# Optimization experiments

Measured on AMD Instinct MI355X. Metric: run time of the kernel, lower is better.

Reference implementation:

```python
import jax, jax.numpy as jnp
import numpy as np

N_NODES = 50000
N_EDGES = 640000
D_IN = 128
D_H1 = 128
D_H2 = 128
N_CLASSES = 64


def setup_inputs() -> dict:
    key = jax.random.key(0)
    ks = jax.random.split(key, 8)
    x = jax.random.normal(ks[0], (N_NODES, D_IN), dtype=jnp.float32)
    edge_index = jax.random.randint(ks[1], (2, N_EDGES), 0, N_NODES, dtype=jnp.int64)
    s1 = 1.0 / np.sqrt(D_IN)
    s2 = 1.0 / np.sqrt(D_H1)
    s3 = 1.0 / np.sqrt(D_H2)
    W1 = jax.random.uniform(ks[2], (D_IN, D_H1), jnp.float32, -s1, s1)
    b1 = jnp.zeros((D_H1,), jnp.float32)
    W2 = jax.random.uniform(ks[3], (D_H1, D_H2), jnp.float32, -s2, s2)
    b2 = jnp.zeros((D_H2,), jnp.float32)
    Wl = jax.random.uniform(ks[4], (D_H2, N_CLASSES), jnp.float32, -s3, s3)
    bl = jax.random.uniform(ks[5], (N_CLASSES,), jnp.float32, -s3, s3)
    return {"x": x, "edge_index": edge_index, "W1": W1, "b1": b1,
            "W2": W2, "b2": b2, "Wl": Wl, "bl": bl}


def _gcn_norm(edge_index, num_nodes):
    # PyG GCNConv: add self-loops, symmetric normalization D^-1/2 (A+I) D^-1/2
    loop = jnp.arange(num_nodes, dtype=edge_index.dtype)
    src = jnp.concatenate([edge_index[0], loop])
    dst = jnp.concatenate([edge_index[1], loop])
    deg = jax.ops.segment_sum(jnp.ones_like(dst, dtype=jnp.float32), dst,
                              num_segments=num_nodes)
    dinv = jnp.where(deg > 0, jax.lax.rsqrt(deg), 0.0)
    norm = dinv[src] * dinv[dst]  # [E+N]
    return src, dst, norm


def _gcn_conv(h, src, dst, norm, W, b, num_nodes):
    h = h @ W                       # transform first (smaller gather when D_out small)
    msg = h[src] * norm[:, None]    # gather + per-edge scale  [E+N, D_out]
    agg = jax.ops.segment_sum(msg, dst, num_segments=num_nodes)  # scatter-add
    return agg + b


def reference(x, edge_index, W1, b1, W2, b2, Wl, bl):
    n = x.shape[0]
    src, dst, norm = _gcn_norm(edge_index, n)
    h = jax.nn.relu(_gcn_conv(x, src, dst, norm, W1, b1, n))
    # dropout is identity in eval mode
    h = jax.nn.relu(_gcn_conv(h, src, dst, norm, W2, b2, n))
    return h @ Wl + bl
```

## Files before the change

### kernel.cpp

```cpp
#include <hip/hip_runtime.h>


typedef __attribute__((ext_vector_type(8))) __bf16 bf16x8;
typedef __attribute__((ext_vector_type(8))) short short8;
typedef __attribute__((ext_vector_type(4))) float f32x4;

__device__ inline float bf_lo(unsigned u) { return __uint_as_float(u << 16); }
__device__ inline float bf_hi(unsigned u) { return __uint_as_float(u & 0xffff0000u); }
__device__ inline unsigned short f2bf(float v) {
  return __builtin_bit_cast(unsigned short, (__bf16)v);
}

__global__ void k_count(const int* __restrict__ dst, int E, int* __restrict__ cnt) {
  int i = blockIdx.x * blockDim.x + threadIdx.x;
  if (i < E) atomicAdd(&cnt[dst[i]], 1);
}

__global__ void k_scan1(const int* __restrict__ cnt, int n, int* __restrict__ partial) {
  __shared__ int s[256];
  int i = blockIdx.x * 256 + threadIdx.x;
  s[threadIdx.x] = (i < n) ? cnt[i] : 0;
  __syncthreads();
  for (int off = 128; off > 0; off >>= 1) {
    if (threadIdx.x < off) s[threadIdx.x] += s[threadIdx.x + off];
    __syncthreads();
  }
  if (threadIdx.x == 0) partial[blockIdx.x] = s[0];
}

__global__ void k_scan3(const int* __restrict__ cnt, const int* __restrict__ partial,
                        int nb, int n, int* __restrict__ row_off, int* __restrict__ cursor,
                        float* __restrict__ dinv) {
  __shared__ int s[256];
  __shared__ int base_s;
  int t = threadIdx.x;
  s[t] = (t < nb && t < (int)blockIdx.x) ? partial[t] : 0;
  __syncthreads();
  for (int off = 128; off > 0; off >>= 1) {
    if (t < off) s[t] += s[t + off];
    __syncthreads();
  }
  if (t == 0) base_s = s[0];
  __syncthreads();
  int base = base_s;
  __syncthreads();

  int i = blockIdx.x * 256 + t;
  int v = (i < n) ? cnt[i] : 0;
  s[t] = v;
  __syncthreads();
  for (int off = 1; off < 256; off <<= 1) {
    int u = (t >= off) ? s[t - off] : 0;
    __syncthreads();
    s[t] += u;
    __syncthreads();
  }
  int incl = s[t];
  int excl = incl - v;
  if (i < n) {
    row_off[i] = base + excl;
    cursor[i] = base + excl;
    dinv[i] = rsqrtf((float)(v + 1));
    if (i == n - 1) row_off[n] = base + incl;
  }
}

__global__ void k_place(const int* __restrict__ src, const int* __restrict__ dst, int E,
                        int* __restrict__ cursor, const float* __restrict__ dinv,
                        unsigned long long* __restrict__ edges) {
  int e = blockIdx.x * blockDim.x + threadIdx.x;
  if (e < E) {
    int s = src[e], d = dst[e];
    int pos = atomicAdd(&cursor[d], 1);
    unsigned long long packed =
        (unsigned long long)(unsigned)s |
        ((unsigned long long)__float_as_uint(dinv[s] * dinv[d]) << 32);
    __builtin_nontemporal_store(packed, &edges[pos]);
  }
}

__global__ void k_prepW(const float* __restrict__ W1, const float* __restrict__ W2,
                        const float* __restrict__ Wl,
                        unsigned short* __restrict__ b1h, unsigned short* __restrict__ b1l,
                        unsigned short* __restrict__ b2h, unsigned short* __restrict__ b2l,
                        unsigned short* __restrict__ blh, unsigned short* __restrict__ bll) {
  int idx = blockIdx.x * 256 + threadIdx.x;
  const float* W;
  unsigned short *bh, *bl_;
  int N, local;
  if (idx < 16384)      { W = W1; bh = b1h; bl_ = b1l; N = 128; local = idx; }
  else if (idx < 32768) { W = W2; bh = b2h; bl_ = b2l; N = 128; local = idx - 16384; }
  else if (idx < 40960) { W = Wl; bh = blh; bl_ = bll; N = 64;  local = idx - 32768; }
  else return;
  int n = local >> 7, k = local & 127;
  float v = W[(size_t)k * N + n];
  __bf16 h = (__bf16)v;
  bh[local] = __builtin_bit_cast(unsigned short, h);
  bl_[local] = f2bf(v - (float)h);
}

template <int NT, bool A32, bool BIAS, bool OUT_BF16>
__global__ __launch_bounds__(256) void gemm2(
    const void* __restrict__ Ahi_, const unsigned short* __restrict__ Alo,
    const unsigned short* __restrict__ Bhi, const unsigned short* __restrict__ Blo,
    const float* __restrict__ bias, void* __restrict__ Cout, int M) {
  constexpr int K = 128;
  constexpr int NCOL = NT * 16;
  __shared__ alignas(16) unsigned short lbh[NCOL * K];
  __shared__ alignas(16) unsigned short lbl[NCOL * K];
  int t = threadIdx.x;
  for (int c = t; c < NCOL * 16; c += 256) {
    int r = c >> 4, q = c & 15;
    int sq = q ^ (r & 15);
    *(short8*)&lbh[r * K + sq * 8] = *(const short8*)&Bhi[r * K + q * 8];
    *(short8*)&lbl[r * K + sq * 8] = *(const short8*)&Blo[r * K + q * 8];
  }
  __syncthreads();

  int lane = t & 63, wave = t >> 6;
  int lm = lane & 15, lk = lane >> 4;
  int m_base = blockIdx.x * 128 + wave * 32;

  f32x4 acc[2][NT] = {};
  const short8 zero8 = {0, 0, 0, 0, 0, 0, 0, 0};

#pragma unroll
  for (int ks = 0; ks < 4; ++ks) {
    int k0 = ks * 32 + lk * 8;
    int chunk = (ks * 4 + lk);
    bf16x8 bh[NT], bl[NT];
#pragma unroll
    for (int nt = 0; nt < NT; ++nt) {
      int r = nt * 16 + lm;
      int sq = chunk ^ lm;
      bh[nt] = *(const bf16x8*)&lbh[r * K + sq * 8];
      bl[nt] = *(const bf16x8*)&lbl[r * K + sq * 8];
    }
#pragma unroll
    for (int mt = 0; mt < 2; ++mt) {
      int row = m_base + mt * 16 + lm;
      bf16x8 ah, al;
      if (A32) {
        const float* Af = (const float*)Ahi_;
        if (row < M) {
          float4 v0 = *(const float4*)&Af[(size_t)row * K + k0];
          float4 v1 = *(const float4*)&Af[(size_t)row * K + k0 + 4];
          float a[8] = {v0.x, v0.y, v0.z, v0.w, v1.x, v1.y, v1.z, v1.w};
#pragma unroll
          for (int j = 0; j < 8; ++j) {
            __bf16 h = (__bf16)a[j];
            ah[j] = h;
            al[j] = (__bf16)(a[j] - (float)h);
          }
        } else {
          ah = __builtin_bit_cast(bf16x8, zero8);
          al = __builtin_bit_cast(bf16x8, zero8);
        }
      } else {
        const unsigned short* Ahi = (const unsigned short*)Ahi_;
        if (row < M) {
          ah = *(const bf16x8*)&Ahi[(size_t)row * K + k0];
          al = *(const bf16x8*)&Alo[(size_t)row * K + k0];
        } else {
          ah = __builtin_bit_cast(bf16x8, zero8);
          al = __builtin_bit_cast(bf16x8, zero8);
        }
      }
#pragma unroll
      for (int nt = 0; nt < NT; ++nt) {
        acc[mt][nt] = __builtin_amdgcn_mfma_f32_16x16x32_bf16(ah, bh[nt], acc[mt][nt], 0, 0, 0);
        acc[mt][nt] = __builtin_amdgcn_mfma_f32_16x16x32_bf16(ah, bl[nt], acc[mt][nt], 0, 0, 0);
        acc[mt][nt] = __builtin_amdgcn_mfma_f32_16x16x32_bf16(al, bh[nt], acc[mt][nt], 0, 0, 0);
      }
    }
  }

#pragma unroll
  for (int mt = 0; mt < 2; ++mt) {
#pragma unroll
    for (int r = 0; r < 4; ++r) {
      int row = m_base + mt * 16 + lk * 4 + r;
      if (row < M) {
#pragma unroll
        for (int nt = 0; nt < NT; ++nt) {
          int col = nt * 16 + lm;
          float v = acc[mt][nt][r];
          if (BIAS) v += bias[col];
          if (OUT_BF16)
            ((unsigned short*)Cout)[(size_t)row * NCOL + col] = f2bf(v);
          else
            ((float*)Cout)[(size_t)row * NCOL + col] = v;
        }
      }
    }
  }
}

__global__ __launch_bounds__(256) void k_agg(const unsigned short* __restrict__ t,
                      const int* __restrict__ row_off,
                      const int2* __restrict__ edges,
                      const float* __restrict__ dinv, const float* __restrict__ bias,
                      unsigned short* __restrict__ ghi, unsigned short* __restrict__ glo,
                      int n) {
  int wave = threadIdx.x >> 6;
  int lane = threadIdx.x & 63;
  int half = lane >> 5;
  int hl = lane & 31;
  int node = blockIdx.x * 4 + wave;
  if (node >= n) return;
  int e0 = row_off[node], e1 = row_off[node + 1];

  float4 a0 = {0,0,0,0}, a1 = {0,0,0,0}, a2 = {0,0,0,0}, a3 = {0,0,0,0};
  int e = e0 + half;
  for (; e + 6 < e1; e += 8) {
    int2 p0 = edges[e],     p1 = edges[e + 2];
    int2 p2 = edges[e + 4], p3 = edges[e + 6];
    uint2 u0 = *(const uint2*)&t[(size_t)p0.x * 128 + hl * 4];
    uint2 u1 = *(const uint2*)&t[(size_t)p1.x * 128 + hl * 4];
    uint2 u2 = *(const uint2*)&t[(size_t)p2.x * 128 + hl * 4];
    uint2 u3 = *(const uint2*)&t[(size_t)p3.x * 128 + hl * 4];
    float w0 = __int_as_float(p0.y), w1 = __int_as_float(p1.y);
    float w2 = __int_as_float(p2.y), w3 = __int_as_float(p3.y);
    a0.x += w0 * bf_lo(u0.x); a0.y += w0 * bf_hi(u0.x);
    a0.z += w0 * bf_lo(u0.y); a0.w += w0 * bf_hi(u0.y);
    a1.x += w1 * bf_lo(u1.x); a1.y += w1 * bf_hi(u1.x);
    a1.z += w1 * bf_lo(u1.y); a1.w += w1 * bf_hi(u1.y);
    a2.x += w2 * bf_lo(u2.x); a2.y += w2 * bf_hi(u2.x);
    a2.z += w2 * bf_lo(u2.y); a2.w += w2 * bf_hi(u2.y);
    a3.x += w3 * bf_lo(u3.x); a3.y += w3 * bf_hi(u3.x);
    a3.z += w3 * bf_lo(u3.y); a3.w += w3 * bf_hi(u3.y);
  }
  for (; e < e1; e += 2) {
    int2 p = edges[e];
    uint2 u = *(const uint2*)&t[(size_t)p.x * 128 + hl * 4];
    float w = __int_as_float(p.y);
    a0.x += w * bf_lo(u.x); a0.y += w * bf_hi(u.x);
    a0.z += w * bf_lo(u.y); a0.w += w * bf_hi(u.y);
  }
  float sx = (a0.x + a1.x) + (a2.x + a3.x);
  float sy = (a0.y + a1.y) + (a2.y + a3.y);
  float sz = (a0.z + a1.z) + (a2.z + a3.z);
  float sw = (a0.w + a1.w) + (a2.w + a3.w);
  sx += __shfl_xor(sx, 32);
  sy += __shfl_xor(sy, 32);
  sz += __shfl_xor(sz, 32);
  sw += __shfl_xor(sw, 32);
  if (half == 0) {
    float di = dinv[node];
    float self = di * di;
    uint2 sv = *(const uint2*)&t[(size_t)node * 128 + hl * 4];
    sx += self * bf_lo(sv.x); sy += self * bf_hi(sv.x);
    sz += self * bf_lo(sv.y); sw += self * bf_hi(sv.y);
    float4 bb = *(const float4*)&bias[hl * 4];
    sx = fmaxf(sx + bb.x, 0.f); sy = fmaxf(sy + bb.y, 0.f);
    sz = fmaxf(sz + bb.z, 0.f); sw = fmaxf(sw + bb.w, 0.f);
    __bf16 hx = (__bf16)sx, hy = (__bf16)sy, hz = (__bf16)sz, hw = (__bf16)sw;
    ushort4 ho, lo;
    ho.x = __builtin_bit_cast(unsigned short, hx);
    ho.y = __builtin_bit_cast(unsigned short, hy);
    ho.z = __builtin_bit_cast(unsigned short, hz);
    ho.w = __builtin_bit_cast(unsigned short, hw);
    lo.x = f2bf(sx - (float)hx);
    lo.y = f2bf(sy - (float)hy);
    lo.z = f2bf(sz - (float)hz);
    lo.w = f2bf(sw - (float)hw);
    *(ushort4*)&ghi[(size_t)node * 128 + hl * 4] = ho;
    *(ushort4*)&glo[(size_t)node * 128 + hl * 4] = lo;
  }
}

extern "C" void kernel_launch(void* const* d_in, const int* in_sizes, int n_in,
                              void* d_out, int out_size, void* d_ws, size_t ws_size,
                              hipStream_t stream) {
  const float* x  = (const float*)d_in[0];
  const int*   ei = (const int*)d_in[1];
  const float* W1 = (const float*)d_in[2];
  const float* b1 = (const float*)d_in[3];
  const float* W2 = (const float*)d_in[4];
  const float* b2 = (const float*)d_in[5];
  const float* Wl = (const float*)d_in[6];
  const float* bl = (const float*)d_in[7];
  float* out = (float*)d_out;

  const int D = 128;
  int N = in_sizes[0] / D;
  int E = in_sizes[1] / 2;
  const int* src = ei;
  const int* dst = ei + E;

  uintptr_t ws = (uintptr_t)d_ws;
  auto take = [&](size_t bytes) {
    uintptr_t p = ws;
    ws += (bytes + 15) & ~(size_t)15;
    return p;
  };
  unsigned short* t_bf = (unsigned short*)take((size_t)N * D * 2);
  unsigned short* xh   = (unsigned short*)take((size_t)N * D * 2);
  unsigned short* xl   = (unsigned short*)take((size_t)N * D * 2);
  unsigned long long* edges = (unsigned long long*)take((size_t)E * 8);
  int*   cnt     = (int*)take((size_t)N * sizeof(int));
  int*   row_off = (int*)take(((size_t)N + 1) * sizeof(int));
  int*   cursor  = (int*)take((size_t)N * sizeof(int));
  float* dinv    = (float*)take((size_t)N * sizeof(float));
  int*   partial = (int*)take(256 * sizeof(int));
  unsigned short* b1h = (unsigned short*)take(128 * 128 * 2);
  unsigned short* b1l = (unsigned short*)take(128 * 128 * 2);
  unsigned short* b2h = (unsigned short*)take(128 * 128 * 2);
  unsigned short* b2l = (unsigned short*)take(128 * 128 * 2);
  unsigned short* blh = (unsigned short*)take(128 * 64 * 2);
  unsigned short* bll = (unsigned short*)take(128 * 64 * 2);

  int nb_n = (N + 255) / 256;
  int nb_e = (E + 255) / 256;

  hipMemsetAsync(cnt, 0, (size_t)N * sizeof(int), stream);
  k_count<<<nb_e, 256, 0, stream>>>(dst, E, cnt);
  k_scan1<<<nb_n, 256, 0, stream>>>(cnt, N, partial);
  k_scan3<<<nb_n, 256, 0, stream>>>(cnt, partial, nb_n, N, row_off, cursor, dinv);
  k_place<<<nb_e, 256, 0, stream>>>(src, dst, E, cursor, dinv, edges);

  k_prepW<<<(40960 + 255) / 256, 256, 0, stream>>>(W1, W2, Wl, b1h, b1l, b2h, b2l, blh, bll);

  int gemm_blocks = (N + 127) / 128;
  int agg_blocks = (N + 3) / 4;

  gemm2<8, true, false, true><<<gemm_blocks, 256, 0, stream>>>(x, nullptr, b1h, b1l, nullptr, t_bf, N);
  k_agg<<<agg_blocks, 256, 0, stream>>>(t_bf, row_off, (const int2*)edges, dinv, b1, xh, xl, N);
  gemm2<8, false, false, true><<<gemm_blocks, 256, 0, stream>>>(xh, xl, b2h, b2l, nullptr, t_bf, N);
  k_agg<<<agg_blocks, 256, 0, stream>>>(t_bf, row_off, (const int2*)edges, dinv, b2, xh, xl, N);
  gemm2<4, false, true, false><<<gemm_blocks, 256, 0, stream>>>(xh, xl, blh, bll, bl, out, N);
}
```

Measured before the change: 260.6 us.

## Prefetch GEMM A tiles, widen aggregation gathers, fuse weight prep into scan

The GEMM now loads all A-operand registers for the whole K extent before staging B into shared memory, so global load latency overlaps the LDS fill. Its final fp32 output uses nontemporal stores. The aggregation kernel is reorganized so each wave processes 4 edge groups of 16 lanes, with each lane gathering 16 bytes (8 bf16) per edge, then reducing across groups with shuffles. Weight preparation is folded into the scan1 launch to drop one kernel launch. Holding more registers for A may reduce occupancy.

```diff
diff --git a/kernel.cpp b/kernel.cpp
--- a/kernel.cpp
+++ b/kernel.cpp
@@ -16,16 +16,38 @@
   if (i < E) atomicAdd(&cnt[dst[i]], 1);
 }
 
-__global__ void k_scan1(const int* __restrict__ cnt, int n, int* __restrict__ partial) {
-  __shared__ int s[256];
-  int i = blockIdx.x * 256 + threadIdx.x;
-  s[threadIdx.x] = (i < n) ? cnt[i] : 0;
-  __syncthreads();
-  for (int off = 128; off > 0; off >>= 1) {
-    if (threadIdx.x < off) s[threadIdx.x] += s[threadIdx.x + off];
+__global__ void k_scan1_prepW(const int* __restrict__ cnt, int n, int* __restrict__ partial,
+                              int nb,
+                              const float* __restrict__ W1, const float* __restrict__ W2,
+                              const float* __restrict__ Wl,
+                              unsigned short* __restrict__ b1h, unsigned short* __restrict__ b1l,
+                              unsigned short* __restrict__ b2h, unsigned short* __restrict__ b2l,
+                              unsigned short* __restrict__ blh, unsigned short* __restrict__ bll) {
+  if ((int)blockIdx.x < nb) {
+    __shared__ int s[256];
+    int i = blockIdx.x * 256 + threadIdx.x;
+    s[threadIdx.x] = (i < n) ? cnt[i] : 0;
     __syncthreads();
-  }
-  if (threadIdx.x == 0) partial[blockIdx.x] = s[0];
+    for (int off = 128; off > 0; off >>= 1) {
+      if (threadIdx.x < off) s[threadIdx.x] += s[threadIdx.x + off];
+      __syncthreads();
+    }
+    if (threadIdx.x == 0) partial[blockIdx.x] = s[0];
+  } else {
+    int idx = ((int)blockIdx.x - nb) * 256 + threadIdx.x;
+    const float* W;
+    unsigned short *bh, *bl_;
+    int N, local;
+    if (idx < 16384)      { W = W1; bh = b1h; bl_ = b1l; N = 128; local = idx; }
+    else if (idx < 32768) { W = W2; bh = b2h; bl_ = b2l; N = 128; local = idx - 16384; }
+    else if (idx < 40960) { W = Wl; bh = blh; bl_ = bll; N = 64;  local = idx - 32768; }
+    else return;
+    int nn = local >> 7, k = local & 127;
+    float v = W[(size_t)k * N + nn];
+    __bf16 h = (__bf16)v;
+    bh[local] = __builtin_bit_cast(unsigned short, h);
+    bl_[local] = f2bf(v - (float)h);
+  }
 }
 
 __global__ void k_scan3(const int* __restrict__ cnt, const int* __restrict__ partial,
@@ -79,28 +101,8 @@
   }
 }
 
-__global__ void k_prepW(const float* __restrict__ W1, const float* __restrict__ W2,
-                        const float* __restrict__ Wl,
-                        unsigned short* __restrict__ b1h, unsigned short* __restrict__ b1l,
-                        unsigned short* __restrict__ b2h, unsigned short* __restrict__ b2l,
-                        unsigned short* __restrict__ blh, unsigned short* __restrict__ bll) {
-  int idx = blockIdx.x * 256 + threadIdx.x;
-  const float* W;
-  unsigned short *bh, *bl_;
-  int N, local;
-  if (idx < 16384)      { W = W1; bh = b1h; bl_ = b1l; N = 128; local = idx; }
-  else if (idx < 32768) { W = W2; bh = b2h; bl_ = b2l; N = 128; local = idx - 16384; }
-  else if (idx < 40960) { W = Wl; bh = blh; bl_ = bll; N = 64;  local = idx - 32768; }
-  else return;
-  int n = local >> 7, k = local & 127;
-  float v = W[(size_t)k * N + n];
-  __bf16 h = (__bf16)v;
-  bh[local] = __builtin_bit_cast(unsigned short, h);
-  bl_[local] = f2bf(v - (float)h);
-}
-
 template <int NT, bool A32, bool BIAS, bool OUT_BF16>
-__global__ __launch_bounds__(256) void gemm2(
+__global__ __launch_bounds__(256) void gemm3(
     const void* __restrict__ Ahi_, const unsigned short* __restrict__ Alo,
     const unsigned short* __restrict__ Bhi, const unsigned short* __restrict__ Blo,
     const float* __restrict__ bias, void* __restrict__ Cout, int M) {
@@ -109,6 +111,60 @@
   __shared__ alignas(16) unsigned short lbh[NCOL * K];
   __shared__ alignas(16) unsigned short lbl[NCOL * K];
   int t = threadIdx.x;
+  int lane = t & 63, wave = t >> 6;
+  int lm = lane & 15, lk = lane >> 4;
+  int m_base = blockIdx.x * 128 + wave * 32;
+  const short8 zero8 = {0, 0, 0, 0, 0, 0, 0, 0};
+
+  bf16x8 ah[2][4], al[2][4];
+  if (A32) {
+    const float* Af = (const float*)Ahi_;
+    float4 ra[2][4][2];
+#pragma unroll
+    for (int mt = 0; mt < 2; ++mt) {
+      int row = m_base + mt * 16 + lm;
+#pragma unroll
+      for (int ks = 0; ks < 4; ++ks) {
+        if (row < M) {
+          ra[mt][ks][0] = *(const float4*)&Af[(size_t)row * K + ks * 32 + lk * 8];
+          ra[mt][ks][1] = *(const float4*)&Af[(size_t)row * K + ks * 32 + lk * 8 + 4];
+        } else {
+          ra[mt][ks][0] = make_float4(0.f, 0.f, 0.f, 0.f);
+          ra[mt][ks][1] = make_float4(0.f, 0.f, 0.f, 0.f);
+        }
+      }
+    }
+#pragma unroll
+    for (int mt = 0; mt < 2; ++mt)
+#pragma unroll
+      for (int ks = 0; ks < 4; ++ks) {
+        float av[8] = {ra[mt][ks][0].x, ra[mt][ks][0].y, ra[mt][ks][0].z, ra[mt][ks][0].w,
+                       ra[mt][ks][1].x, ra[mt][ks][1].y, ra[mt][ks][1].z, ra[mt][ks][1].w};
+#pragma unroll
+        for (int j = 0; j < 8; ++j) {
+          __bf16 h = (__bf16)av[j];
+          ah[mt][ks][j] = h;
+          al[mt][ks][j] = (__bf16)(av[j] - (float)h);
+        }
+      }
+  } else {
+    const unsigned short* Ahi = (const unsigned short*)Ahi_;
+#pragma unroll
+    for (int mt = 0; mt < 2; ++mt) {
+      int row = m_base + mt * 16 + lm;
+#pragma unroll
+      for (int ks = 0; ks < 4; ++ks) {
+        if (row < M) {
+          ah[mt][ks] = *(const bf16x8*)&Ahi[(size_t)row * K + ks * 32 + lk * 8];
+          al[mt][ks] = *(const bf16x8*)&Alo[(size_t)row * K + ks * 32 + lk * 8];
+        } else {
+          ah[mt][ks] = __builtin_bit_cast(bf16x8, zero8);
+          al[mt][ks] = __builtin_bit_cast(bf16x8, zero8);
+        }
+      }
+    }
+  }
+
   for (int c = t; c < NCOL * 16; c += 256) {
     int r = c >> 4, q = c & 15;
     int sq = q ^ (r & 15);
@@ -117,17 +173,10 @@
   }
   __syncthreads();
 
-  int lane = t & 63, wave = t >> 6;
-  int lm = lane & 15, lk = lane >> 4;
-  int m_base = blockIdx.x * 128 + wave * 32;
-
   f32x4 acc[2][NT] = {};
-  const short8 zero8 = {0, 0, 0, 0, 0, 0, 0, 0};
-
 #pragma unroll
   for (int ks = 0; ks < 4; ++ks) {
-    int k0 = ks * 32 + lk * 8;
-    int chunk = (ks * 4 + lk);
+    int chunk = ks * 4 + lk;
     bf16x8 bh[NT], bl[NT];
 #pragma unroll
     for (int nt = 0; nt < NT; ++nt) {
@@ -137,42 +186,13 @@
       bl[nt] = *(const bf16x8*)&lbl[r * K + sq * 8];
     }
 #pragma unroll
-    for (int mt = 0; mt < 2; ++mt) {
-      int row = m_base + mt * 16 + lm;
-      bf16x8 ah, al;
-      if (A32) {
-        const float* Af = (const float*)Ahi_;
-        if (row < M) {
-          float4 v0 = *(const float4*)&Af[(size_t)row * K + k0];
-          float4 v1 = *(const float4*)&Af[(size_t)row * K + k0 + 4];
-          float a[8] = {v0.x, v0.y, v0.z, v0.w, v1.x, v1.y, v1.z, v1.w};
-#pragma unroll
-          for (int j = 0; j < 8; ++j) {
-            __bf16 h = (__bf16)a[j];
-            ah[j] = h;
-            al[j] = (__bf16)(a[j] - (float)h);
-          }
-        } else {
-          ah = __builtin_bit_cast(bf16x8, zero8);
-          al = __builtin_bit_cast(bf16x8, zero8);
-        }
-      } else {
-        const unsigned short* Ahi = (const unsigned short*)Ahi_;
-        if (row < M) {
-          ah = *(const bf16x8*)&Ahi[(size_t)row * K + k0];
-          al = *(const bf16x8*)&Alo[(size_t)row * K + k0];
-        } else {
-          ah = __builtin_bit_cast(bf16x8, zero8);
-          al = __builtin_bit_cast(bf16x8, zero8);
-        }
-      }
+    for (int mt = 0; mt < 2; ++mt)
 #pragma unroll
       for (int nt = 0; nt < NT; ++nt) {
-        acc[mt][nt] = __builtin_amdgcn_mfma_f32_16x16x32_bf16(ah, bh[nt], acc[mt][nt], 0, 0, 0);
-        acc[mt][nt] = __builtin_amdgcn_mfma_f32_16x16x32_bf16(ah, bl[nt], acc[mt][nt], 0, 0, 0);
-        acc[mt][nt] = __builtin_amdgcn_mfma_f32_16x16x32_bf16(al, bh[nt], acc[mt][nt], 0, 0, 0);
-      }
-    }
+        acc[mt][nt] = __builtin_amdgcn_mfma_f32_16x16x32_bf16(ah[mt][ks], bh[nt], acc[mt][nt], 0, 0, 0);
+        acc[mt][nt] = __builtin_amdgcn_mfma_f32_16x16x32_bf16(ah[mt][ks], bl[nt], acc[mt][nt], 0, 0, 0);
+        acc[mt][nt] = __builtin_amdgcn_mfma_f32_16x16x32_bf16(al[mt][ks], bh[nt], acc[mt][nt], 0, 0, 0);
+      }
   }
 
 #pragma unroll
@@ -189,7 +209,7 @@
           if (OUT_BF16)
             ((unsigned short*)Cout)[(size_t)row * NCOL + col] = f2bf(v);
           else
-            ((float*)Cout)[(size_t)row * NCOL + col] = v;
+            __builtin_nontemporal_store(v, &((float*)Cout)[(size_t)row * NCOL + col]);
         }
       }
     }
@@ -204,68 +224,59 @@
                       int n) {
   int wave = threadIdx.x >> 6;
   int lane = threadIdx.x & 63;
-  int half = lane >> 5;
-  int hl = lane & 31;
+  int g = lane >> 4;
+  int fl = lane & 15;
   int node = blockIdx.x * 4 + wave;
   if (node >= n) return;
   int e0 = row_off[node], e1 = row_off[node + 1];
-
-  float4 a0 = {0,0,0,0}, a1 = {0,0,0,0}, a2 = {0,0,0,0}, a3 = {0,0,0,0};
-  int e = e0 + half;
-  for (; e + 6 < e1; e += 8) {
-    int2 p0 = edges[e],     p1 = edges[e + 2];
-    int2 p2 = edges[e + 4], p3 = edges[e + 6];
-    uint2 u0 = *(const uint2*)&t[(size_t)p0.x * 128 + hl * 4];
-    uint2 u1 = *(const uint2*)&t[(size_t)p1.x * 128 + hl * 4];
-    uint2 u2 = *(const uint2*)&t[(size_t)p2.x * 128 + hl * 4];
-    uint2 u3 = *(const uint2*)&t[(size_t)p3.x * 128 + hl * 4];
-    float w0 = __int_as_float(p0.y), w1 = __int_as_float(p1.y);
-    float w2 = __int_as_float(p2.y), w3 = __int_as_float(p3.y);
-    a0.x += w0 * bf_lo(u0.x); a0.y += w0 * bf_hi(u0.x);
-    a0.z += w0 * bf_lo(u0.y); a0.w += w0 * bf_hi(u0.y);
-    a1.x += w1 * bf_lo(u1.x); a1.y += w1 * bf_hi(u1.x);
-    a1.z += w1 * bf_lo(u1.y); a1.w += w1 * bf_hi(u1.y);
-    a2.x += w2 * bf_lo(u2.x); a2.y += w2 * bf_hi(u2.x);
-    a2.z += w2 * bf_lo(u2.y); a2.w += w2 * bf_hi(u2.y);
-    a3.x += w3 * bf_lo(u3.x); a3.y += w3 * bf_hi(u3.x);
-    a3.z += w3 * bf_lo(u3.y); a3.w += w3 * bf_hi(u3.y);
-  }
-  for (; e < e1; e += 2) {
-    int2 p = edges[e];
-    uint2 u = *(const uint2*)&t[(size_t)p.x * 128 + hl * 4];
-    float w = __int_as_float(p.y);
-    a0.x += w * bf_lo(u.x); a0.y += w * bf_hi(u.x);
-    a0.z += w * bf_lo(u.y); a0.w += w * bf_hi(u.y);
-  }
-  float sx = (a0.x + a1.x) + (a2.x + a3.x);
-  float sy = (a0.y + a1.y) + (a2.y + a3.y);
-  float sz = (a0.z + a1.z) + (a2.z + a3.z);
-  float sw = (a0.w + a1.w) + (a2.w + a3.w);
-  sx += __shfl_xor(sx, 32);
-  sy += __shfl_xor(sy, 32);
-  sz += __shfl_xor(sz, 32);
-  sw += __shfl_xor(sw, 32);
-  if (half == 0) {
+  int last = e1 - 1;
+
+  float acc[8] = {};
+  for (int base = e0; base < e1; base += 8) {
+    int i0 = base + g, i1 = base + 4 + g;
+    int c0 = i0 < e1 ? i0 : last;
+    int c1 = i1 < e1 ? i1 : last;
+    int2 p0 = edges[c0];
+    int2 p1 = edges[c1];
+    uint4 u0 = *(const uint4*)&t[(size_t)p0.x * 128 + fl * 8];
+    uint4 u1 = *(const uint4*)&t[(size_t)p1.x * 128 + fl * 8];
+    float w0 = i0 < e1 ? __int_as_float(p0.y) : 0.f;
+    float w1 = i1 < e1 ? __int_as_float(p1.y) : 0.f;
+    acc[0] += w0 * bf_lo(u0.x); acc[1] += w0 * bf_hi(u0.x);
+    acc[2] += w0 * bf_lo(u0.y); acc[3] += w0 * bf_hi(u0.y);
+    acc[4] += w0 * bf_lo(u0.z); acc[5] += w0 * bf_hi(u0.z);
+    acc[6] += w0 * bf_lo(u0.w); acc[7] += w0 * bf_hi(u0.w);
+    acc[0] += w1 * bf_lo(u1.x); acc[1] += w1 * bf_hi(u1.x);
+    acc[2] += w1 * bf_lo(u1.y); acc[3] += w1 * bf_hi(u1.y);
+    acc[4] += w1 * bf_lo(u1.z); acc[5] += w1 * bf_hi(u1.z);
+    acc[6] += w1 * bf_lo(u1.w); acc[7] += w1 * bf_hi(u1.w);
+  }
+#pragma unroll
+  for (int j = 0; j < 8; ++j) {
+    acc[j] += __shfl_xor(acc[j], 16);
+    acc[j] += __shfl_xor(acc[j], 32);
+  }
+  if (g == 0) {
     float di = dinv[node];
     float self = di * di;
-    uint2 sv = *(const uint2*)&t[(size_t)node * 128 + hl * 4];
-    sx += self * bf_lo(sv.x); sy += self * bf_hi(sv.x);
-    sz += self * bf_lo(sv.y); sw += self * bf_hi(sv.y);
-    float4 bb = *(const float4*)&bias[hl * 4];
-    sx = fmaxf(sx + bb.x, 0.f); sy = fmaxf(sy + bb.y, 0.f);
-    sz = fmaxf(sz + bb.z, 0.f); sw = fmaxf(sw + bb.w, 0.f);
-    __bf16 hx = (__bf16)sx, hy = (__bf16)sy, hz = (__bf16)sz, hw = (__bf16)sw;
-    ushort4 ho, lo;
-    ho.x = __builtin_bit_cast(unsigned short, hx);
-    ho.y = __builtin_bit_cast(unsigned short, hy);
-    ho.z = __builtin_bit_cast(unsigned short, hz);
-    ho.w = __builtin_bit_cast(unsigned short, hw);
-    lo.x = f2bf(sx - (float)hx);
-    lo.y = f2bf(sy - (float)hy);
-    lo.z = f2bf(sz - (float)hz);
-    lo.w = f2bf(sw - (float)hw);
-    *(ushort4*)&ghi[(size_t)node * 128 + hl * 4] = ho;
-    *(ushort4*)&glo[(size_t)node * 128 + hl * 4] = lo;
+    uint4 sv = *(const uint4*)&t[(size_t)node * 128 + fl * 8];
+    acc[0] += self * bf_lo(sv.x); acc[1] += self * bf_hi(sv.x);
+    acc[2] += self * bf_lo(sv.y); acc[3] += self * bf_hi(sv.y);
+    acc[4] += self * bf_lo(sv.z); acc[5] += self * bf_hi(sv.z);
+    acc[6] += self * bf_lo(sv.w); acc[7] += self * bf_hi(sv.w);
+    float4 bb0 = *(const float4*)&bias[fl * 8];
+    float4 bb1 = *(const float4*)&bias[fl * 8 + 4];
+    float bb[8] = {bb0.x, bb0.y, bb0.z, bb0.w, bb1.x, bb1.y, bb1.z, bb1.w};
+    short8 ho, lo_;
+#pragma unroll
+    for (int j = 0; j < 8; ++j) {
+      float s = fmaxf(acc[j] + bb[j], 0.f);
+      __bf16 h = (__bf16)s;
+      ho[j] = __builtin_bit_cast(short, h);
+      lo_[j] = (short)f2bf(s - (float)h);
+    }
+    *(short8*)&ghi[(size_t)node * 128 + fl * 8] = ho;
+    *(short8*)&glo[(size_t)node * 128 + fl * 8] = lo_;
   }
 }
 
@@ -315,18 +326,17 @@
 
   hipMemsetAsync(cnt, 0, (size_t)N * sizeof(int), stream);
   k_count<<<nb_e, 256, 0, stream>>>(dst, E, cnt);
-  k_scan1<<<nb_n, 256, 0, stream>>>(cnt, N, partial);
+  k_scan1_prepW<<<nb_n + 160, 256, 0, stream>>>(cnt, N, partial, nb_n,
+                                                W1, W2, Wl, b1h, b1l, b2h, b2l, blh, bll);
   k_scan3<<<nb_n, 256, 0, stream>>>(cnt, partial, nb_n, N, row_off, cursor, dinv);
   k_place<<<nb_e, 256, 0, stream>>>(src, dst, E, cursor, dinv, edges);
 
-  k_prepW<<<(40960 + 255) / 256, 256, 0, stream>>>(W1, W2, Wl, b1h, b1l, b2h, b2l, blh, bll);
-
   int gemm_blocks = (N + 127) / 128;
   int agg_blocks = (N + 3) / 4;
 
-  gemm2<8, true, false, true><<<gemm_blocks, 256, 0, stream>>>(x, nullptr, b1h, b1l, nullptr, t_bf, N);
+  gemm3<8, true, false, true><<<gemm_blocks, 256, 0, stream>>>(x, nullptr, b1h, b1l, nullptr, t_bf, N);
   k_agg<<<agg_blocks, 256, 0, stream>>>(t_bf, row_off, (const int2*)edges, dinv, b1, xh, xl, N);
-  gemm2<8, false, false, true><<<gemm_blocks, 256, 0, stream>>>(xh, xl, b2h, b2l, nullptr, t_bf, N);
+  gemm3<8, false, false, true><<<gemm_blocks, 256, 0, stream>>>(xh, xl, b2h, b2l, nullptr, t_bf, N);
   k_agg<<<agg_blocks, 256, 0, stream>>>(t_bf, row_off, (const int2*)edges, dinv, b2, xh, xl, N);
-  gemm2<4, false, true, false><<<gemm_blocks, 256, 0, stream>>>(xh, xl, blh, bll, bl, out, N);
-}
+  gemm3<4, false, true, false><<<gemm_blocks, 256, 0, stream>>>(xh, xl, blh, bll, bl, out, N);
+}
```

Measured after the change: 246.5 us. -5.4%, faster.
